# Kernel optimization log

Hardware: AMD Instinct MI355X
Metric: run time of the kernel (lower is better)

The kernel has to match this reference:

```python
import jax, jax.numpy as jnp
import numpy as np

N, IN_C, HID, OUT_C, DEPTH = 4096, 128, 256, 128, 3
KS = [2048, 1024, 512]  # ceil(0.5 * N_level)
E = 131072


def glorot(key, fan_in, fan_out):
    lim = np.sqrt(6.0 / (fan_in + fan_out))
    return jax.random.uniform(key, (fan_in, fan_out), jnp.float32, -lim, lim)


def build_adj(edge_index, n):
    # symmetric, self-loop-free adjacency with unit edge weights
    A = jnp.zeros((n, n), jnp.float32)
    A = A.at[edge_index[0], edge_index[1]].set(1.0)
    A = jnp.maximum(A, A.T)
    return A * (1.0 - jnp.eye(n, dtype=jnp.float32))


def gcn(x, A, W, b):
    # GCNConv(improved=True): A_hat = A + 2I, symmetric normalization
    n = A.shape[0]
    Ah = A + 2.0 * jnp.eye(n, dtype=A.dtype)
    deg = Ah.sum(axis=1)
    dinv = jnp.where(deg > 0, deg ** -0.5, 0.0)
    An = dinv[:, None] * Ah * dinv[None, :]
    return An @ (x @ W) + b


def augment(A):
    # remove self loops, add self loops (w=1), square (spspmm), remove self loops
    n = A.shape[0]
    I = jnp.eye(n, dtype=A.dtype)
    Al = A * (1.0 - I) + I
    A2 = Al @ Al
    return A2 * (1.0 - I)


def topk_pool(x, A, p, k):
    score = jnp.tanh((x @ p) / jnp.linalg.norm(p))
    vals, perm = jax.lax.top_k(score, k)
    return x[perm] * vals[:, None], A[perm][:, perm], perm


def setup_inputs() -> dict:
    key = jax.random.key(0)
    ks = jax.random.split(key, 16)
    x = jax.random.normal(ks[0], (N, IN_C), jnp.float32)
    edge_index = jax.random.randint(ks[1], (2, E), 0, N, jnp.int32)
    d = {"x": x, "edge_index": edge_index}
    d["Wd0"], d["bd0"] = glorot(ks[2], IN_C, HID), jnp.zeros((HID,), jnp.float32)
    d["Wd1"], d["bd1"] = glorot(ks[3], HID, HID), jnp.zeros((HID,), jnp.float32)
    d["Wd2"], d["bd2"] = glorot(ks[4], HID, HID), jnp.zeros((HID,), jnp.float32)
    d["Wd3"], d["bd3"] = glorot(ks[5], HID, HID), jnp.zeros((HID,), jnp.float32)
    d["p1"] = jax.random.normal(ks[6], (HID,), jnp.float32)
    d["p2"] = jax.random.normal(ks[7], (HID,), jnp.float32)
    d["p3"] = jax.random.normal(ks[8], (HID,), jnp.float32)
    d["Wu0"], d["bu0"] = glorot(ks[9], HID, HID), jnp.zeros((HID,), jnp.float32)
    d["Wu1"], d["bu1"] = glorot(ks[10], HID, HID), jnp.zeros((HID,), jnp.float32)
    d["Wu2"], d["bu2"] = glorot(ks[11], HID, OUT_C), jnp.zeros((OUT_C,), jnp.float32)
    return d


def reference(x, edge_index, Wd0, bd0, Wd1, bd1, Wd2, bd2, Wd3, bd3,
              p1, p2, p3, Wu0, bu0, Wu1, bu1, Wu2, bu2):
    n = x.shape[0]
    A = build_adj(edge_index, n)
    x = jax.nn.relu(gcn(x, A, Wd0, bd0))
    xs, As, perms = [x], [A], []
    down = [(Wd1, bd1), (Wd2, bd2), (Wd3, bd3)]
    pools = [p1, p2, p3]
    for i in range(DEPTH):
        A = augment(A)
        x, A, perm = topk_pool(x, A, pools[i], KS[i])
        x = jax.nn.relu(gcn(x, A, *down[i]))
        if i < DEPTH - 1:
            xs.append(x)
            As.append(A)
        perms.append(perm)
    up = [(Wu0, bu0), (Wu1, bu1), (Wu2, bu2)]
    for i in range(DEPTH):
        j = DEPTH - 1 - i
        res, perm = xs[j], perms[j]
        u = jnp.zeros_like(res).at[perm].set(x)
        x = res + u  # sum_res=True
        x = gcn(x, As[j], *up[i])
        if i < DEPTH - 1:
            x = jax.nn.relu(x)
    return x
```

## Files before the change

kernel.cpp:

```cpp
#include <hip/hip_runtime.h>


typedef __attribute__((ext_vector_type(8))) short bf16x8;
typedef __attribute__((ext_vector_type(4))) short s16x4;
typedef __attribute__((ext_vector_type(4))) float f32x4;

__device__ __forceinline__ short f2bf(float f) {
    unsigned u = __builtin_bit_cast(unsigned, f);
    u += 0x7FFFu + ((u >> 16) & 1u);
    return (short)(u >> 16);
}
__device__ __forceinline__ float bf2f(short s) {
    unsigned u = ((unsigned)(unsigned short)s) << 16;
    return __builtin_bit_cast(float, u);
}

#define GLL16(gsrc, ldst)                                                        \
    __builtin_amdgcn_global_load_lds(                                            \
        (__attribute__((address_space(1))) void*)(gsrc),                         \
        (__attribute__((address_space(3))) void*)(ldst), 16, 0, 0)

template<int MODE, int EPI>
__global__ __launch_bounds__(256, 2)
void gemm_bt(const short* __restrict__ Ah, const short* __restrict__ Al,
             const short* __restrict__ Bh, const short* __restrict__ Bl,
             float* __restrict__ Cf, int M, int N, int K, int kChunk)
{
    if (EPI == 1 && (int)blockIdx.y > (int)blockIdx.x) return;

    __shared__ short sAh[128 * 32];
    __shared__ short sBh[128 * 32];
    __shared__ short sAl[(MODE == 2) ? 128 * 32 : 8];
    __shared__ short sBl[(MODE >= 1) ? 128 * 32 : 8];

    const int t    = threadIdx.x;
    const int lane = t & 63;
    const int wave = t >> 6;
    const int tM   = blockIdx.y * 128;
    const int tN   = blockIdx.x * 128;
    const int k0   = blockIdx.z * kChunk;

    const int wm  = (wave >> 1) * 64;
    const int wn  = (wave & 1) * 64;
    const int l15 = lane & 15;
    const int g8  = (lane >> 4) * 8;

    f32x4 acc[4][4];
    const f32x4 zero = {0.f, 0.f, 0.f, 0.f};
#pragma unroll
    for (int i = 0; i < 4; i++)
#pragma unroll
        for (int j = 0; j < 4; j++) acc[i][j] = zero;

    const int i0 = t, i1 = t + 256;
    const short* a0 = Ah + (size_t)(tM + (i0 >> 2)) * K + (i0 & 3) * 8;
    const short* a1 = Ah + (size_t)(tM + (i1 >> 2)) * K + (i1 & 3) * 8;
    const short* b0 = Bh + (size_t)(tN + (i0 >> 2)) * K + (i0 & 3) * 8;
    const short* b1 = Bh + (size_t)(tN + (i1 >> 2)) * K + (i1 & 3) * 8;
    const short *bl0 = nullptr, *bl1 = nullptr, *al0 = nullptr, *al1 = nullptr;
    if (MODE >= 1) {
        bl0 = Bl + (size_t)(tN + (i0 >> 2)) * K + (i0 & 3) * 8;
        bl1 = Bl + (size_t)(tN + (i1 >> 2)) * K + (i1 & 3) * 8;
    }
    if (MODE == 2) {
        al0 = Al + (size_t)(tM + (i0 >> 2)) * K + (i0 & 3) * 8;
        al1 = Al + (size_t)(tM + (i1 >> 2)) * K + (i1 & 3) * 8;
    }

    for (int kb = k0; kb < k0 + kChunk; kb += 32) {
        GLL16(a0 + kb, &sAh[i0 * 8]);
        GLL16(a1 + kb, &sAh[i1 * 8]);
        GLL16(b0 + kb, &sBh[i0 * 8]);
        GLL16(b1 + kb, &sBh[i1 * 8]);
        if (MODE >= 1) { GLL16(bl0 + kb, &sBl[i0 * 8]); GLL16(bl1 + kb, &sBl[i1 * 8]); }
        if (MODE == 2) { GLL16(al0 + kb, &sAl[i0 * 8]); GLL16(al1 + kb, &sAl[i1 * 8]); }
        __syncthreads();

        bf16x8 aF[4], bF[4], aL[4], bL[4];
#pragma unroll
        for (int i = 0; i < 4; i++)
            aF[i] = *(const bf16x8*)&sAh[(wm + i * 16 + l15) * 32 + g8];
#pragma unroll
        for (int j = 0; j < 4; j++)
            bF[j] = *(const bf16x8*)&sBh[(wn + j * 16 + l15) * 32 + g8];
        if (MODE >= 1)
#pragma unroll
            for (int j = 0; j < 4; j++)
                bL[j] = *(const bf16x8*)&sBl[(wn + j * 16 + l15) * 32 + g8];
        if (MODE == 2)
#pragma unroll
            for (int i = 0; i < 4; i++)
                aL[i] = *(const bf16x8*)&sAl[(wm + i * 16 + l15) * 32 + g8];

#pragma unroll
        for (int i = 0; i < 4; i++)
#pragma unroll
            for (int j = 0; j < 4; j++) {
                acc[i][j] = __builtin_amdgcn_mfma_f32_16x16x32_bf16(aF[i], bF[j], acc[i][j], 0, 0, 0);
                if (MODE >= 1)
                    acc[i][j] = __builtin_amdgcn_mfma_f32_16x16x32_bf16(aF[i], bL[j], acc[i][j], 0, 0, 0);
                if (MODE == 2)
                    acc[i][j] = __builtin_amdgcn_mfma_f32_16x16x32_bf16(aL[i], bF[j], acc[i][j], 0, 0, 0);
            }
        __syncthreads();
    }

    const int r4 = (lane >> 4) * 4;
    if (EPI == 3) {
        float* CT = Cf + (size_t)blockIdx.z * M * N;
#pragma unroll
        for (int i = 0; i < 4; i++)
#pragma unroll
            for (int j = 0; j < 4; j++) {
                const int col   = tN + wn + j * 16 + l15;
                const int rbase = tM + wm + i * 16 + r4;
                *(f32x4*)&CT[(size_t)col * M + rbase] = acc[i][j];
            }
    } else {
        float* Cg = Cf + (size_t)blockIdx.z * M * N;
#pragma unroll
        for (int i = 0; i < 4; i++)
#pragma unroll
            for (int j = 0; j < 4; j++) {
                const int col = tN + wn + j * 16 + l15;
                float* cp = Cg + (size_t)(tM + wm + i * 16 + r4) * N + col;
#pragma unroll
                for (int r = 0; r < 4; r++) cp[(size_t)r * N] = acc[i][j][r];
            }
        if (EPI == 1 && tM != tN) {
#pragma unroll
            for (int i = 0; i < 4; i++)
#pragma unroll
                for (int j = 0; j < 4; j++) {
                    const int col   = tN + wn + j * 16 + l15;
                    const int rbase = tM + wm + i * 16 + r4;
                    *(f32x4*)&Cg[(size_t)col * N + rbase] = acc[i][j];
                }
        }
    }
}


__global__ void prep(const float* __restrict__ Wd0, const float* __restrict__ Wd1,
                     const float* __restrict__ Wd2, const float* __restrict__ Wd3,
                     const float* __restrict__ Wu0, const float* __restrict__ Wu1,
                     const float* __restrict__ Wu2, const float* __restrict__ x0,
                     short* __restrict__ Wth, short* __restrict__ Wtl,
                     short* __restrict__ Xh, short* __restrict__ Xl)
{
    int t = blockIdx.x * 256 + threadIdx.x;
    float v; int dst;
    if (t < 32768)       { int e = t;          v = Wd0[e]; dst = 0      + (e & 255) * 128 + (e >> 8); }
    else if (t < 98304)  { int e = t - 32768;  v = Wd1[e]; dst = 32768  + (e & 255) * 256 + (e >> 8); }
    else if (t < 163840) { int e = t - 98304;  v = Wd2[e]; dst = 98304  + (e & 255) * 256 + (e >> 8); }
    else if (t < 229376) { int e = t - 163840; v = Wd3[e]; dst = 163840 + (e & 255) * 256 + (e >> 8); }
    else if (t < 294912) { int e = t - 229376; v = Wu0[e]; dst = 229376 + (e & 255) * 256 + (e >> 8); }
    else if (t < 360448) { int e = t - 294912; v = Wu1[e]; dst = 294912 + (e & 255) * 256 + (e >> 8); }
    else if (t < 393216) { int e = t - 360448; v = Wu2[e]; dst = 360448 + (e & 127) * 256 + (e >> 7); }
    else {
        int e = t - 393216;
        v = x0[e];
        short h = f2bf(v);
        Xh[e] = h; Xl[e] = f2bf(v - bf2f(h));
        return;
    }
    short h = f2bf(v);
    Wth[dst] = h; Wtl[dst] = f2bf(v - bf2f(h));
}

__global__ void build_adj_bf16(const int* __restrict__ ei, int E,
                               short* __restrict__ A, int n)
{
    int e = blockIdx.x * 256 + threadIdx.x;
    if (e >= E) return;
    int i = ei[e], j = ei[E + e];
    if (i != j) {
        A[(size_t)i * n + j] = (short)0x3F80;
        A[(size_t)j * n + i] = (short)0x3F80;
    }
}

__global__ void row_compact(const short* __restrict__ A, int n,
                            int* __restrict__ csr, float* __restrict__ rs)
{
    int row = blockIdx.x * 4 + (threadIdx.x >> 6);
    int lane = threadIdx.x & 63;
    const short* ar = A + (size_t)row * n;
    int* out = csr + (size_t)row * 128;
    int base = 0;
    for (int c0 = 0; c0 < n; c0 += 64) {
        short v = ar[c0 + lane];
        unsigned long long mask = __ballot(v != 0);
        if (v != 0) {
            int pos = base + __popcll(mask & ((1ull << lane) - 1ull));
            if (pos < 128) out[pos] = c0 + lane;
        }
        base += __popcll(mask);
    }
    if (lane == 0) rs[row] = (float)base;
}

__global__ void build_mask(const int* __restrict__ csr, const float* __restrict__ deg,
                           const int* __restrict__ perm,
                           unsigned long long* __restrict__ mask,
                           float* __restrict__ rs)
{
    __shared__ unsigned long long m[4][64];
    int wave = threadIdx.x >> 6, lane = threadIdx.x & 63;
    int r = blockIdx.x * 4 + wave;
    int u = perm[r];
    m[wave][lane] = 0ull;
    __syncthreads();
    int dg = (int)deg[u];
    const int* nb = csr + (size_t)u * 128;
    for (int q = lane; q < dg; q += 64) {
        int c = nb[q];
        atomicOr(&m[wave][c >> 6], 1ull << (c & 63));
    }
    if (lane == 0) {
        atomicOr(&m[wave][u >> 6], 1ull << (u & 63));
        rs[r] = 0.f;
    }
    __syncthreads();
    mask[(size_t)r * 64 + lane] = m[wave][lane];
}

#define PSTR2 18
__global__ __launch_bounds__(256, 8)
void popc_aug_p(const unsigned long long* __restrict__ mask,
                short* __restrict__ Cp)
{
    const int bx = blockIdx.x, by = blockIdx.y, z = blockIdx.z;
    if (by > bx) return;
    __shared__ unsigned long long a[64 * PSTR2];
    __shared__ unsigned long long b[64 * PSTR2];
    const int t = threadIdx.x;
#pragma unroll
    for (int p = 0; p < 4; p++) {
        int idx = p * 256 + t;
        int rr = idx >> 4, w = idx & 15;
        a[rr * PSTR2 + w] = mask[((size_t)(by * 64 + rr)) * 64 + z * 16 + w];
        b[rr * PSTR2 + w] = mask[((size_t)(bx * 64 + rr)) * 64 + z * 16 + w];
    }
    __syncthreads();
    const int i0 = (t >> 4) * 4;
    const int j0 = t & 15;
    int acc[4][4];
#pragma unroll
    for (int qi = 0; qi < 4; qi++)
#pragma unroll
        for (int qj = 0; qj < 4; qj++) acc[qi][qj] = 0;
#pragma unroll
    for (int w = 0; w < 16; w += 2) {
        ulong2 av[4], bv[4];
#pragma unroll
        for (int q = 0; q < 4; q++) av[q] = *(const ulong2*)&a[(i0 + q) * PSTR2 + w];
#pragma unroll
        for (int q = 0; q < 4; q++) bv[q] = *(const ulong2*)&b[(j0 + 16 * q) * PSTR2 + w];
#pragma unroll
        for (int qi = 0; qi < 4; qi++)
#pragma unroll
            for (int qj = 0; qj < 4; qj++) {
                acc[qi][qj] += __builtin_popcountll(av[qi].x & bv[qj].x);
                acc[qi][qj] += __builtin_popcountll(av[qi].y & bv[qj].y);
            }
    }
    short* out = Cp + ((size_t)z * 1024 + (size_t)(by * 32 + bx)) * 4096;
#pragma unroll
    for (int qi = 0; qi < 4; qi++)
#pragma unroll
        for (int qj = 0; qj < 4; qj++)
            out[(i0 + qi) * 64 + j0 + 16 * qj] = (short)acc[qi][qj];
}

__global__ __launch_bounds__(256)
void aug_merge(const short* __restrict__ Cp, int kk,
               short* __restrict__ Ahs, float* __restrict__ rs)
{
    const int bx = blockIdx.x, by = blockIdx.y;
    if (by > bx) return;
    __shared__ float tile[64][65];
    __shared__ float rsum[64], csum[64];
    const int t = threadIdx.x;
    const int i  = t >> 2;
    const int c0 = (t & 3) * 16;
    const size_t tb = (size_t)(by * 32 + bx) * 4096;
    const size_t ss = (size_t)1024 * 4096;
    if (t < 64) { rsum[t] = 0.f; csum[t] = 0.f; }

    int v[16];
#pragma unroll
    for (int q = 0; q < 16; q++) v[q] = 0;
    for (int s = 0; s < 4; s++) {
        bf16x8 p0 = *(const bf16x8*)&Cp[tb + s * ss + i * 64 + c0];
        bf16x8 p1 = *(const bf16x8*)&Cp[tb + s * ss + i * 64 + c0 + 8];
#pragma unroll
        for (int q = 0; q < 8; q++) { v[q] += (int)p0[q]; v[8 + q] += (int)p1[q]; }
    }
    const int gi = by * 64 + i;
    float rp = 0.f;
    s16x4 pk[4];
#pragma unroll
    for (int q = 0; q < 16; q++) {
        const int gj = bx * 64 + c0 + q;
        float val = (gi == gj) ? 0.f : (float)v[q];
        tile[i][c0 + q] = val;
        rp += val;
        pk[q >> 2][q & 3] = f2bf(val);
    }
#pragma unroll
    for (int q = 0; q < 4; q++)
        *(s16x4*)&Ahs[(size_t)gi * kk + bx * 64 + c0 + q * 4] = pk[q];
    __syncthreads();
    atomicAdd(&rsum[i], rp);
    if (bx != by) {
        float cpv = 0.f;
#pragma unroll
        for (int q = 0; q < 16; q++) {
            float val = tile[c0 + q][i];
            cpv += val;
            pk[q >> 2][q & 3] = f2bf(val);
        }
#pragma unroll
        for (int q = 0; q < 4; q++)
            *(s16x4*)&Ahs[(size_t)(bx * 64 + i) * kk + by * 64 + c0 + q * 4] = pk[q];
        atomicAdd(&csum[i], cpv);
    }
    __syncthreads();
    if (t < 64) {
        atomicAdd(&rs[by * 64 + t], rsum[t]);
        if (bx != by) atomicAdd(&rs[bx * 64 + t], csum[t]);
    }
}

__global__ void z_reduce(const float* __restrict__ Cp, int S,
                         const float* __restrict__ rs,
                         short* __restrict__ Zh, short* __restrict__ Zl,
                         int n, int C)
{
    int t4 = (blockIdx.x * 256 + threadIdx.x) * 4;
    int r = t4 % n;
    size_t stride = (size_t)n * C;
    f32x4 v = {0.f, 0.f, 0.f, 0.f};
    for (int s = 0; s < S; s++) v += *(const f32x4*)&Cp[t4 + s * stride];
    f32x4 rsv = *(const f32x4*)&rs[r];
    s16x4 zh, zl;
#pragma unroll
    for (int q = 0; q < 4; q++) {
        float z = v[q] / sqrtf(rsv[q] + 2.f);
        short h = f2bf(z);
        zh[q] = h; zl[q] = f2bf(z - bf2f(h));
    }
    *(s16x4*)&Zh[t4] = zh;
    *(s16x4*)&Zl[t4] = zl;
}

__global__ void zf_reduce(const float* __restrict__ Cp, int S,
                          const float* __restrict__ rs,
                          float* __restrict__ Zf, int n, int C)
{
    int t4 = (blockIdx.x * 256 + threadIdx.x) * 4;
    int r = t4 / C;
    size_t stride = (size_t)n * C;
    f32x4 v = {0.f, 0.f, 0.f, 0.f};
    for (int s = 0; s < S; s++) v += *(const f32x4*)&Cp[t4 + s * stride];
    float d = 1.f / sqrtf(rs[r] + 2.f);
    v *= d;
    *(f32x4*)&Zf[t4] = v;
}

template<int CN, int RELU>
__global__ __launch_bounds__(256)
void spmm_gcn(const int* __restrict__ csr, const float* __restrict__ rs,
              const float* __restrict__ Zf, const float* __restrict__ b,
              float* __restrict__ out)
{
    const int lane = threadIdx.x & 63;
    const int row  = blockIdx.x * 4 + (threadIdx.x >> 6);
    const int dg   = (int)rs[row];
    const int* nb  = csr + (size_t)row * 128;
    if (CN == 256) {
        const int c = lane * 4;
        float4 acc = {0.f, 0.f, 0.f, 0.f};
        int q = 0;
        for (; q + 4 <= dg; q += 4) {
            int j0 = nb[q], j1 = nb[q+1], j2 = nb[q+2], j3 = nb[q+3];
            float4 z0 = *(const float4*)&Zf[(size_t)j0 * CN + c];
            float4 z1 = *(const float4*)&Zf[(size_t)j1 * CN + c];
            float4 z2 = *(const float4*)&Zf[(size_t)j2 * CN + c];
            float4 z3 = *(const float4*)&Zf[(size_t)j3 * CN + c];
            acc.x += z0.x; acc.y += z0.y; acc.z += z0.z; acc.w += z0.w;
            acc.x += z1.x; acc.y += z1.y; acc.z += z1.z; acc.w += z1.w;
            acc.x += z2.x; acc.y += z2.y; acc.z += z2.z; acc.w += z2.w;
            acc.x += z3.x; acc.y += z3.y; acc.z += z3.z; acc.w += z3.w;
        }
        for (; q < dg; q++) {
            float4 z = *(const float4*)&Zf[(size_t)nb[q] * CN + c];
            acc.x += z.x; acc.y += z.y; acc.z += z.z; acc.w += z.w;
        }
        float d = 1.f / sqrtf(rs[row] + 2.f);
        float4 zi = *(const float4*)&Zf[(size_t)row * CN + c];
        float4 bb = *(const float4*)&b[c];
        float4 g;
        g.x = d * acc.x + 2.f * d * zi.x + bb.x;
        g.y = d * acc.y + 2.f * d * zi.y + bb.y;
        g.z = d * acc.z + 2.f * d * zi.z + bb.z;
        g.w = d * acc.w + 2.f * d * zi.w + bb.w;
        if (RELU) {
            g.x = fmaxf(g.x, 0.f); g.y = fmaxf(g.y, 0.f);
            g.z = fmaxf(g.z, 0.f); g.w = fmaxf(g.w, 0.f);
        }
        *(float4*)&out[(size_t)row * CN + c] = g;
    } else {
        const int c = lane * 2;
        float2 acc = {0.f, 0.f};
        int q = 0;
        for (; q + 4 <= dg; q += 4) {
            int j0 = nb[q], j1 = nb[q+1], j2 = nb[q+2], j3 = nb[q+3];
            float2 z0 = *(const float2*)&Zf[(size_t)j0 * CN + c];
            float2 z1 = *(const float2*)&Zf[(size_t)j1 * CN + c];
            float2 z2 = *(const float2*)&Zf[(size_t)j2 * CN + c];
            float2 z3 = *(const float2*)&Zf[(size_t)j3 * CN + c];
            acc.x += z0.x; acc.y += z0.y;
            acc.x += z1.x; acc.y += z1.y;
            acc.x += z2.x; acc.y += z2.y;
            acc.x += z3.x; acc.y += z3.y;
        }
        for (; q < dg; q++) {
            float2 z = *(const float2*)&Zf[(size_t)nb[q] * CN + c];
            acc.x += z.x; acc.y += z.y;
        }
        float d = 1.f / sqrtf(rs[row] + 2.f);
        float2 zi = *(const float2*)&Zf[(size_t)row * CN + c];
        float2 g;
        g.x = d * acc.x + 2.f * d * zi.x + b[c];
        g.y = d * acc.y + 2.f * d * zi.y + b[c + 1];
        if (RELU) { g.x = fmaxf(g.x, 0.f); g.y = fmaxf(g.y, 0.f); }
        *(float2*)&out[(size_t)row * CN + c] = g;
    }
}

__global__ void gcn_final(const float* __restrict__ Cp, int S,
                          const short* __restrict__ Zh, const short* __restrict__ Zl,
                          const float* __restrict__ rs, const float* __restrict__ b,
                          float* __restrict__ out, short* __restrict__ oh,
                          short* __restrict__ ol, int k, int C, int relu,
                          const int* __restrict__ inv, const float* __restrict__ res)
{
    int t4 = (blockIdx.x * 256 + threadIdx.x) * 4;
    int j = t4 / C, c = t4 - j * C;
    int r = inv ? inv[j] : j;
    f32x4 v = res ? *(const f32x4*)&res[t4] : (f32x4){0.f, 0.f, 0.f, 0.f};
    if (r >= 0) {
        size_t base = (size_t)r * C + c;
        size_t stride = (size_t)k * C;
        f32x4 az = {0.f, 0.f, 0.f, 0.f};
        for (int s = 0; s < S; s++) az += *(const f32x4*)&Cp[base + s * stride];
        float d = 1.f / sqrtf(rs[r] + 2.f);
        f32x4 bb = *(const f32x4*)&b[c];
#pragma unroll
        for (int q = 0; q < 4; q++) {
            size_t zi = (size_t)(c + q) * k + r;
            float zz = bf2f(Zh[zi]) + bf2f(Zl[zi]);
            float g = d * az[q] + 2.f * d * zz + bb[q];
            if (relu && g < 0.f) g = 0.f;
            v[q] += g;
        }
    }
    *(f32x4*)&out[t4] = v;
    if (oh) {
        s16x4 hh, ll;
#pragma unroll
        for (int q = 0; q < 4; q++) {
            short h = f2bf(v[q]);
            hh[q] = h; ll[q] = f2bf(v[q] - bf2f(h));
        }
        *(s16x4*)&oh[t4] = hh;
        *(s16x4*)&ol[t4] = ll;
    }
}

__global__ void score_kernel(const float* __restrict__ x,
                             const float* __restrict__ p,
                             float* __restrict__ score, int n,
                             int* __restrict__ rankb)
{
    int row = blockIdx.x * 4 + (threadIdx.x >> 6);
    int lane = threadIdx.x & 63;
    float4 pv = ((const float4*)p)[lane];
    float4 xv = ((const float4*)(x + (size_t)row * 256))[lane];
    double nn  = (double)pv.x * pv.x + (double)pv.y * pv.y +
                 (double)pv.z * pv.z + (double)pv.w * pv.w;
    double acc = (double)xv.x * pv.x + (double)xv.y * pv.y +
                 (double)xv.z * pv.z + (double)xv.w * pv.w;
    for (int off = 32; off; off >>= 1) {
        acc += __shfl_down(acc, off);
        nn  += __shfl_down(nn, off);
    }
    if (lane == 0) {
        score[row] = tanhf((float)(acc / sqrt(nn)));
        rankb[row] = 0;
    }
}

__device__ __forceinline__ unsigned long long packkey(float s, int i) {
    unsigned u = __builtin_bit_cast(unsigned, s);
    u = (u & 0x80000000u) ? ~u : (u | 0x80000000u);
    return ((unsigned long long)u << 32) | (unsigned)(0xFFFFFFFFu - (unsigned)i);
}

__global__ __launch_bounds__(256)
void rank_count(const float* __restrict__ score,
                int* __restrict__ rankb)
{
    __shared__ unsigned long long sk[256];
    int i = blockIdx.x * 256 + threadIdx.x;
    int j = blockIdx.y * 256 + threadIdx.x;
    sk[threadIdx.x] = packkey(score[j], j);
    unsigned long long mykey = packkey(score[i], i);
    __syncthreads();
    int part = 0;
#pragma unroll 16
    for (int q = 0; q < 256; q++) part += (sk[q] > mykey) ? 1 : 0;
    atomicAdd(&rankb[i], part);
}

__global__ void rank_final(const float* __restrict__ score,
                           const int* __restrict__ rankb, int k,
                           int* __restrict__ perm, float* __restrict__ vals,
                           int* __restrict__ inv)
{
    int i = blockIdx.x * 256 + threadIdx.x;
    int rank = rankb[i];
    if (rank < k) { perm[rank] = i; vals[rank] = score[i]; }
    inv[i] = (rank < k) ? rank : -1;
}

__global__ void gather_x_hl(const float* __restrict__ xold,
                            const int* __restrict__ perm,
                            const float* __restrict__ vals,
                            short* __restrict__ Xh, short* __restrict__ Xl, int C)
{
    int t4 = (blockIdx.x * 256 + threadIdx.x) * 4;
    int r = t4 / C, c = t4 - r * C;
    float vv = vals[r];
    f32x4 x = *(const f32x4*)&xold[(size_t)perm[r] * C + c];
    s16x4 hh, ll;
#pragma unroll
    for (int q = 0; q < 4; q++) {
        float v = x[q] * vv;
        short h = f2bf(v);
        hh[q] = h; ll[q] = f2bf(v - bf2f(h));
    }
    *(s16x4*)&Xh[t4] = hh;
    *(s16x4*)&Xl[t4] = ll;
}

__global__ void gatherG_h(const short* __restrict__ A, int n,
                          const int* __restrict__ perm,
                          short* __restrict__ Gh, int kk,
                          float* __restrict__ rsz)
{
    int idx = blockIdx.x * 256 + threadIdx.x;
    if (idx < kk) rsz[idx] = 0.f;
    int t8 = idx * 8;
    if (t8 >= kk * n) return;
    int r = t8 / n, c0 = t8 - r * n;
    int pr = perm[r];
    bf16x8 a = *(const bf16x8*)&A[(size_t)pr * n + c0];
    if (pr >= c0 && pr < c0 + 8)
        a[pr - c0] = f2bf(bf2f(a[pr - c0]) + 1.f);
    *(bf16x8*)&Gh[t8] = a;
}

__global__ void gatherG_hl(const short* __restrict__ Ahi, const short* __restrict__ Alo,
                           int n, const int* __restrict__ perm,
                           short* __restrict__ Gh, short* __restrict__ Gl, int kk,
                           float* __restrict__ rsz)
{
    int idx = blockIdx.x * 256 + threadIdx.x;
    if (idx < kk) rsz[idx] = 0.f;
    int t8 = idx * 8;
    if (t8 >= kk * n) return;
    int r = t8 / n, c0 = t8 - r * n;
    int pr = perm[r];
    bf16x8 ah = *(const bf16x8*)&Ahi[(size_t)pr * n + c0];
    bf16x8 al = *(const bf16x8*)&Alo[(size_t)pr * n + c0];
    bf16x8 gh, gl;
#pragma unroll
    for (int q = 0; q < 8; q++) {
        float v = bf2f(ah[q]) + bf2f(al[q]) + ((c0 + q == pr) ? 1.f : 0.f);
        short h = f2bf(v);
        gh[q] = h; gl[q] = f2bf(v - bf2f(h));
    }
    *(bf16x8*)&Gh[t8] = gh;
    *(bf16x8*)&Gl[t8] = gl;
}

template<bool LO>
__global__ void aug_finish_f(const float* __restrict__ Cp, int S, int kk,
                             short* __restrict__ Ahs, short* __restrict__ Als,
                             float* __restrict__ rs)
{
    int t4 = (blockIdx.x * 256 + threadIdx.x) * 4;
    int r = t4 / kk, c0 = t4 - r * kk;
    size_t stride = (size_t)kk * kk;
    f32x4 v = {0.f, 0.f, 0.f, 0.f};
    for (int s = 0; s < S; s++) v += *(const f32x4*)&Cp[t4 + s * stride];
    if (r >= c0 && r < c0 + 4) v[r - c0] = 0.f;
    s16x4 hh, ll;
    float ws = 0.f;
#pragma unroll
    for (int q = 0; q < 4; q++) {
        short h = f2bf(v[q]);
        hh[q] = h;
        if (LO) ll[q] = f2bf(v[q] - bf2f(h));
        ws += v[q];
    }
    *(s16x4*)&Ahs[t4] = hh;
    if (LO) *(s16x4*)&Als[t4] = ll;
    for (int off = 32; off; off >>= 1) ws += __shfl_down(ws, off);
    if ((threadIdx.x & 63) == 0) atomicAdd(&rs[r], ws);
}


extern "C" void kernel_launch(void* const* d_in, const int* in_sizes, int n_in,
                              void* d_out, int out_size, void* d_ws, size_t ws_size,
                              hipStream_t stream)
{
    const float* x0  = (const float*)d_in[0];
    const int*   ei  = (const int*)d_in[1];
    const float* Wd0 = (const float*)d_in[2];  const float* bd0 = (const float*)d_in[3];
    const float* Wd1 = (const float*)d_in[4];  const float* bd1 = (const float*)d_in[5];
    const float* Wd2 = (const float*)d_in[6];  const float* bd2 = (const float*)d_in[7];
    const float* Wd3 = (const float*)d_in[8];  const float* bd3 = (const float*)d_in[9];
    const float* p1  = (const float*)d_in[10];
    const float* p2  = (const float*)d_in[11];
    const float* p3  = (const float*)d_in[12];
    const float* Wu0 = (const float*)d_in[13]; const float* bu0 = (const float*)d_in[14];
    const float* Wu1 = (const float*)d_in[15]; const float* bu1 = (const float*)d_in[16];
    const float* Wu2 = (const float*)d_in[17]; const float* bu2 = (const float*)d_in[18];

    const int E = in_sizes[1] / 2;

    char* ws = (char*)d_ws;
    size_t off = 0;
    auto alloc = [&](size_t bytes) -> void* {
        void* p = ws + off;
        off += (bytes + 255) & ~(size_t)255;
        return p;
    };
    short* A0h  = (short*)alloc((size_t)4096 * 4096 * 2);
    short* A1h  = (short*)alloc((size_t)2048 * 2048 * 2);
    short* A2h  = (short*)alloc((size_t)1024 * 1024 * 2);
    short* A2l  = (short*)alloc((size_t)1024 * 1024 * 2);
    short* A3h  = (short*)alloc((size_t)512 * 512 * 2);
    short* A3l  = (short*)alloc((size_t)512 * 512 * 2);
    short* Gh   = (short*)alloc((size_t)1024 * 2048 * 2);
    short* Gl   = (short*)alloc((size_t)512 * 1024 * 2);
    int*   csr  = (int*)alloc((size_t)4096 * 128 * 4);
    unsigned long long* maskb = (unsigned long long*)alloc((size_t)2048 * 64 * 8);
    float* Zf   = (float*)alloc((size_t)4096 * 256 * 4);
    float* Cp   = (float*)alloc((size_t)64 * 1024 * 1024);
    float* xs0  = (float*)alloc((size_t)4096 * 256 * 4);
    float* xs1  = (float*)alloc((size_t)2048 * 256 * 4);
    float* xs2  = (float*)alloc((size_t)1024 * 256 * 4);
    float* xu0  = (float*)alloc((size_t)4096 * 256 * 4);
    float* xu1  = (float*)alloc((size_t)2048 * 256 * 4);
    float* xu2  = (float*)alloc((size_t)1024 * 256 * 4);
    short* xu0h = (short*)alloc((size_t)4096 * 256 * 2);
    short* xu0l = (short*)alloc((size_t)4096 * 256 * 2);
    short* xu1h = (short*)alloc((size_t)2048 * 256 * 2);
    short* xu1l = (short*)alloc((size_t)2048 * 256 * 2);
    short* xu2h = (short*)alloc((size_t)1024 * 256 * 2);
    short* xu2l = (short*)alloc((size_t)1024 * 256 * 2);
    short* X0h  = (short*)alloc((size_t)4096 * 128 * 2);
    short* X0l  = (short*)alloc((size_t)4096 * 128 * 2);
    short* xah  = (short*)alloc((size_t)2048 * 256 * 2);
    short* xal  = (short*)alloc((size_t)2048 * 256 * 2);
    short* Wth  = (short*)alloc((size_t)393216 * 2);
    short* Wtl  = (short*)alloc((size_t)393216 * 2);
    short* Zh   = (short*)alloc((size_t)256 * 4096 * 2);
    short* Zl   = (short*)alloc((size_t)256 * 4096 * 2);
    float* rs0  = (float*)alloc(4096 * 4);
    float* rs1  = (float*)alloc(2048 * 4);
    float* rs2  = (float*)alloc(1024 * 4);
    float* rs3  = (float*)alloc(512 * 4);
    float* scoreb = (float*)alloc(4096 * 4);
    float* valsb  = (float*)alloc(2048 * 4);
    int*   rankb  = (int*)alloc(4096 * 4);
    int*   perm1  = (int*)alloc(2048 * 4);
    int*   perm2  = (int*)alloc(1024 * 4);
    int*   perm3  = (int*)alloc(512 * 4);
    int*   inv1   = (int*)alloc(4096 * 4);
    int*   inv2   = (int*)alloc(2048 * 4);
    int*   inv3   = (int*)alloc(1024 * 4);

    auto gcn_dense = [&](const short* Xh, const short* Xl, int n, int Kc, int Cout,
                         const short* pAh, const short* pAl, const float* rsA,
                         int wtoff, const float* b,
                         float* out, short* oh, short* ol, int relu, int modeA,
                         int Saz, const int* inv, const float* res, int nout) {
        int Sxw = 4;
        gemm_bt<2, 3><<<dim3(Cout / 128, n / 128, Sxw), 256, 0, stream>>>(
            Xh, Xl, Wth + wtoff, Wtl + wtoff, Cp, n, Cout, Kc, Kc / Sxw);
        z_reduce<<<(n * Cout) / 1024, 256, 0, stream>>>(Cp, Sxw, rsA, Zh, Zl, n, Cout);
        dim3 g(Cout / 128, n / 128, Saz);
        if (modeA == 1)
            gemm_bt<1, 0><<<g, 256, 0, stream>>>(pAh, nullptr, Zh, Zl, Cp, n, Cout, n, n / Saz);
        else
            gemm_bt<2, 0><<<g, 256, 0, stream>>>(pAh, pAl, Zh, Zl, Cp, n, Cout, n, n / Saz);
        gcn_final<<<(nout * Cout) / 1024, 256, 0, stream>>>(
            Cp, Saz, Zh, Zl, rsA, b, out, oh, ol, n, Cout, relu, inv, res);
    };

    auto pool = [&](const float* xlev, int n, const float* p, int* perm, int* inv) {
        int k = n / 2;
        score_kernel<<<n / 4, 256, 0, stream>>>(xlev, p, scoreb, n, rankb);
        rank_count<<<dim3(n / 256, n / 256), 256, 0, stream>>>(scoreb, rankb);
        rank_final<<<n / 256, 256, 0, stream>>>(scoreb, rankb, k, perm, valsb, inv);
        gather_x_hl<<<k / 4, 256, 0, stream>>>(xlev, perm, valsb, xah, xal, 256);
    };

    prep<<<3584, 256, 0, stream>>>(Wd0, Wd1, Wd2, Wd3, Wu0, Wu1, Wu2, x0,
                                   Wth, Wtl, X0h, X0l);
    hipMemsetAsync(A0h, 0, (size_t)4096 * 4096 * 2, stream);
    build_adj_bf16<<<(E + 255) / 256, 256, 0, stream>>>(ei, E, A0h, 4096);
    row_compact<<<1024, 256, 0, stream>>>(A0h, 4096, csr, rs0);

    gemm_bt<2, 0><<<dim3(2, 32, 4), 256, 0, stream>>>(
        X0h, X0l, Wth, Wtl, Cp, 4096, 256, 128, 32);
    zf_reduce<<<1024, 256, 0, stream>>>(Cp, 4, rs0, Zf, 4096, 256);
    spmm_gcn<256, 1><<<1024, 256, 0, stream>>>(csr, rs0, Zf, bd0, xs0);

    pool(xs0, 4096, p1, perm1, inv1);
    build_mask<<<512, 256, 0, stream>>>(csr, rs0, perm1, maskb, rs1);
    popc_aug_p<<<dim3(32, 32, 4), 256, 0, stream>>>(maskb, (short*)Cp);
    aug_merge<<<dim3(32, 32), 256, 0, stream>>>((const short*)Cp, 2048, A1h, rs1);
    gcn_dense(xah, xal, 2048, 256, 256, A1h, nullptr, rs1, 32768, bd1,
              xs1, nullptr, nullptr, 1, 1, 16, nullptr, nullptr, 2048);

    pool(xs1, 2048, p2, perm2, inv2);
    gatherG_h<<<(1024 * 2048 / 8) / 256, 256, 0, stream>>>(A1h, 2048, perm2, Gh, 1024, rs2);
    gemm_bt<0, 1><<<dim3(8, 8, 8), 256, 0, stream>>>(Gh, nullptr, Gh, nullptr, Cp, 1024, 1024, 2048, 256);
    aug_finish_f<true><<<(1024 * 1024 / 4) / 256, 256, 0, stream>>>(Cp, 8, 1024, A2h, A2l, rs2);
    gcn_dense(xah, xal, 1024, 256, 256, A2h, A2l, rs2, 98304, bd2,
              xs2, nullptr, nullptr, 1, 2, 8, nullptr, nullptr, 1024);

    pool(xs2, 1024, p3, perm3, inv3);
    gatherG_hl<<<(512 * 1024 / 8) / 256, 256, 0, stream>>>(A2h, A2l, 1024, perm3, Gh, Gl, 512, rs3);
    gemm_bt<2, 1><<<dim3(4, 4, 8), 256, 0, stream>>>(Gh, Gl, Gh, Gl, Cp, 512, 512, 1024, 128);
    aug_finish_f<true><<<(512 * 512 / 4) / 256, 256, 0, stream>>>(Cp, 8, 512, A3h, A3l, rs3);

    gcn_dense(xah, xal, 512, 256, 256, A3h, A3l, rs3, 163840, bd3,
              xu2, xu2h, xu2l, 1, 2, 8, inv3, xs2, 1024);

    gcn_dense(xu2h, xu2l, 1024, 256, 256, A2h, A2l, rs2, 229376, bu0,
              xu1, xu1h, xu1l, 1, 2, 8, inv2, xs1, 2048);

    gcn_dense(xu1h, xu1l, 2048, 256, 256, A1h, nullptr, rs1, 294912, bu1,
              xu0, xu0h, xu0l, 1, 1, 16, inv1, xs0, 4096);

    gemm_bt<2, 0><<<dim3(1, 32, 8), 256, 0, stream>>>(
        xu0h, xu0l, Wth + 360448, Wtl + 360448, Cp, 4096, 128, 256, 32);
    zf_reduce<<<512, 256, 0, stream>>>(Cp, 8, rs0, Zf, 4096, 128);
    spmm_gcn<128, 0><<<1024, 256, 0, stream>>>(csr, rs0, Zf, bu2, (float*)d_out);
}
```

Measured before the change: 466.3 us.

## Replace dense bf16 level-0 adjacency with a bitmask and derive CSR and masks from bits

The 4096x4096 bf16 adjacency matrix (32 MB memset, scatter and full row scan) is replaced by a 4096x64 uint64 bitmask. Zeroing the bitmask is folded into the prep kernel, and edges are set with atomicOr. CSR rows are built by a per-row popcount prefix scan, and the pooled mask for the first augmentation is gathered straight from the bitmask instead of rebuilt from the CSR. The split-K factor for two level-1 dense GCNs also drops from 16 to 8. The change avoids a large memory footprint and bandwidth cost, at the price of global 64-bit atomics on the bitmask.

Result: faster. 443.9 us (-4.8%).

```diff
diff --git a/kernel.cpp b/kernel.cpp
--- a/kernel.cpp
+++ b/kernel.cpp
@@ -146,7 +146,8 @@
                      const float* __restrict__ Wu0, const float* __restrict__ Wu1,
                      const float* __restrict__ Wu2, const float* __restrict__ x0,
                      short* __restrict__ Wth, short* __restrict__ Wtl,
-                     short* __restrict__ Xh, short* __restrict__ Xl)
+                     short* __restrict__ Xh, short* __restrict__ Xl,
+                     unsigned long long* __restrict__ M0)
 {
     int t = blockIdx.x * 256 + threadIdx.x;
     float v; int dst;
@@ -157,72 +158,67 @@
     else if (t < 294912) { int e = t - 229376; v = Wu0[e]; dst = 229376 + (e & 255) * 256 + (e >> 8); }
     else if (t < 360448) { int e = t - 294912; v = Wu1[e]; dst = 294912 + (e & 255) * 256 + (e >> 8); }
     else if (t < 393216) { int e = t - 360448; v = Wu2[e]; dst = 360448 + (e & 127) * 256 + (e >> 7); }
-    else {
+    else if (t < 917504) {
         int e = t - 393216;
         v = x0[e];
         short h = f2bf(v);
         Xh[e] = h; Xl[e] = f2bf(v - bf2f(h));
         return;
+    } else {
+        M0[t - 917504] = 0ull;
+        return;
     }
     short h = f2bf(v);
     Wth[dst] = h; Wtl[dst] = f2bf(v - bf2f(h));
 }
 
-__global__ void build_adj_bf16(const int* __restrict__ ei, int E,
-                               short* __restrict__ A, int n)
+__global__ void build_bits(const int* __restrict__ ei, int E,
+                           unsigned long long* __restrict__ M0)
 {
     int e = blockIdx.x * 256 + threadIdx.x;
     if (e >= E) return;
     int i = ei[e], j = ei[E + e];
     if (i != j) {
-        A[(size_t)i * n + j] = (short)0x3F80;
-        A[(size_t)j * n + i] = (short)0x3F80;
-    }
-}
-
-__global__ void row_compact(const short* __restrict__ A, int n,
-                            int* __restrict__ csr, float* __restrict__ rs)
+        atomicOr(&M0[(size_t)i * 64 + (j >> 6)], 1ull << (j & 63));
+        atomicOr(&M0[(size_t)j * 64 + (i >> 6)], 1ull << (i & 63));
+    }
+}
+
+__global__ void row_compact_bits(const unsigned long long* __restrict__ M0,
+                                 int* __restrict__ csr, float* __restrict__ rs)
 {
     int row = blockIdx.x * 4 + (threadIdx.x >> 6);
     int lane = threadIdx.x & 63;
-    const short* ar = A + (size_t)row * n;
+    unsigned long long w = M0[(size_t)row * 64 + lane];
+    int c = __popcll(w);
+    int incl = c;
+    for (int off = 1; off < 64; off <<= 1) {
+        int v = __shfl_up(incl, off);
+        if (lane >= off) incl += v;
+    }
+    int base = incl - c;
     int* out = csr + (size_t)row * 128;
-    int base = 0;
-    for (int c0 = 0; c0 < n; c0 += 64) {
-        short v = ar[c0 + lane];
-        unsigned long long mask = __ballot(v != 0);
-        if (v != 0) {
-            int pos = base + __popcll(mask & ((1ull << lane) - 1ull));
-            if (pos < 128) out[pos] = c0 + lane;
-        }
-        base += __popcll(mask);
-    }
-    if (lane == 0) rs[row] = (float)base;
-}
-
-__global__ void build_mask(const int* __restrict__ csr, const float* __restrict__ deg,
-                           const int* __restrict__ perm,
-                           unsigned long long* __restrict__ mask,
-                           float* __restrict__ rs)
-{
-    __shared__ unsigned long long m[4][64];
-    int wave = threadIdx.x >> 6, lane = threadIdx.x & 63;
-    int r = blockIdx.x * 4 + wave;
+    while (w) {
+        int b = __ffsll((unsigned long long)w) - 1;
+        if (base < 128) out[base] = lane * 64 + b;
+        base++;
+        w &= w - 1;
+    }
+    if (lane == 63) rs[row] = (float)incl;
+}
+
+__global__ void mask_gather(const unsigned long long* __restrict__ M0,
+                            const int* __restrict__ perm,
+                            unsigned long long* __restrict__ mask,
+                            float* __restrict__ rs, int kk)
+{
+    int t = blockIdx.x * 256 + threadIdx.x;
+    if (t < kk) rs[t] = 0.f;
+    int r = t >> 6, l = t & 63;
     int u = perm[r];
-    m[wave][lane] = 0ull;
-    __syncthreads();
-    int dg = (int)deg[u];
-    const int* nb = csr + (size_t)u * 128;
-    for (int q = lane; q < dg; q += 64) {
-        int c = nb[q];
-        atomicOr(&m[wave][c >> 6], 1ull << (c & 63));
-    }
-    if (lane == 0) {
-        atomicOr(&m[wave][u >> 6], 1ull << (u & 63));
-        rs[r] = 0.f;
-    }
-    __syncthreads();
-    mask[(size_t)r * 64 + lane] = m[wave][lane];
+    unsigned long long w = M0[(size_t)u * 64 + l];
+    if ((u >> 6) == l) w |= 1ull << (u & 63);
+    mask[t] = w;
 }
 
 #define PSTR2 18
@@ -650,7 +646,7 @@
         off += (bytes + 255) & ~(size_t)255;
         return p;
     };
-    short* A0h  = (short*)alloc((size_t)4096 * 4096 * 2);
+    unsigned long long* M0 = (unsigned long long*)alloc((size_t)4096 * 64 * 8);
     short* A1h  = (short*)alloc((size_t)2048 * 2048 * 2);
     short* A2h  = (short*)alloc((size_t)1024 * 1024 * 2);
     short* A2l  = (short*)alloc((size_t)1024 * 1024 * 2);
@@ -722,11 +718,10 @@
         gather_x_hl<<<k / 4, 256, 0, stream>>>(xlev, perm, valsb, xah, xal, 256);
     };
 
-    prep<<<3584, 256, 0, stream>>>(Wd0, Wd1, Wd2, Wd3, Wu0, Wu1, Wu2, x0,
-                                   Wth, Wtl, X0h, X0l);
-    hipMemsetAsync(A0h, 0, (size_t)4096 * 4096 * 2, stream);
-    build_adj_bf16<<<(E + 255) / 256, 256, 0, stream>>>(ei, E, A0h, 4096);
-    row_compact<<<1024, 256, 0, stream>>>(A0h, 4096, csr, rs0);
+    prep<<<4608, 256, 0, stream>>>(Wd0, Wd1, Wd2, Wd3, Wu0, Wu1, Wu2, x0,
+                                   Wth, Wtl, X0h, X0l, M0);
+    build_bits<<<(E + 255) / 256, 256, 0, stream>>>(ei, E, M0);
+    row_compact_bits<<<1024, 256, 0, stream>>>(M0, csr, rs0);
 
     gemm_bt<2, 0><<<dim3(2, 32, 4), 256, 0, stream>>>(
         X0h, X0l, Wth, Wtl, Cp, 4096, 256, 128, 32);
@@ -734,11 +729,11 @@
     spmm_gcn<256, 1><<<1024, 256, 0, stream>>>(csr, rs0, Zf, bd0, xs0);
 
     pool(xs0, 4096, p1, perm1, inv1);
-    build_mask<<<512, 256, 0, stream>>>(csr, rs0, perm1, maskb, rs1);
+    mask_gather<<<512, 256, 0, stream>>>(M0, perm1, maskb, rs1, 2048);
     popc_aug_p<<<dim3(32, 32, 4), 256, 0, stream>>>(maskb, (short*)Cp);
     aug_merge<<<dim3(32, 32), 256, 0, stream>>>((const short*)Cp, 2048, A1h, rs1);
     gcn_dense(xah, xal, 2048, 256, 256, A1h, nullptr, rs1, 32768, bd1,
-              xs1, nullptr, nullptr, 1, 1, 16, nullptr, nullptr, 2048);
+              xs1, nullptr, nullptr, 1, 1, 8, nullptr, nullptr, 2048);
 
     pool(xs1, 2048, p2, perm2, inv2);
     gatherG_h<<<(1024 * 2048 / 8) / 256, 256, 0, stream>>>(A1h, 2048, perm2, Gh, 1024, rs2);
@@ -759,7 +754,7 @@
               xu1, xu1h, xu1l, 1, 2, 8, inv2, xs1, 2048);
 
     gcn_dense(xu1h, xu1l, 2048, 256, 256, A1h, nullptr, rs1, 294912, bu1,
-              xu0, xu0h, xu0l, 1, 1, 16, inv1, xs0, 4096);
+              xu0, xu0h, xu0l, 1, 1, 8, inv1, xs0, 4096);
 
     gemm_bt<2, 0><<<dim3(1, 32, 8), 256, 0, stream>>>(
         xu0h, xu0l, Wth + 360448, Wtl + 360448, Cp, 4096, 128, 256, 32);
```
